# Optimization experiments

Measured on AMD Instinct MI355X. Metric: run time of the kernel, lower is better.

## Reference

```python
import jax, jax.numpy as jnp
import numpy as np

B, T, D = 4, 2048, 2048
HS, NH, NG = 128, 16, 4  # head_size, n_head, n_query_groups
R = NH // NG             # queries per group


def setup_inputs() -> dict:
    key = jax.random.key(0)
    ks = jax.random.split(key, 8)
    s = 0.02
    return {
        "x": jax.random.normal(ks[0], (B, T, D), dtype=jnp.float32),
        "WQ": jax.random.normal(ks[1], (HS * NH, D), dtype=jnp.float32) * s,
        "bQ": jax.random.normal(ks[2], (HS * NH,), dtype=jnp.float32) * s,
        "WK": jax.random.normal(ks[3], (HS * NG, D), dtype=jnp.float32) * s,
        "bK": jax.random.normal(ks[4], (HS * NG,), dtype=jnp.float32) * s,
        "WV": jax.random.normal(ks[5], (HS * NG, D), dtype=jnp.float32) * s,
        "bV": jax.random.normal(ks[6], (HS * NG,), dtype=jnp.float32) * s,
        "proj": jax.random.normal(ks[7], (HS * NH, D), dtype=jnp.float32) * s,
    }


def reference(x, WQ, bQ, WK, bK, WV, bV, proj):
    b, t, _ = x.shape
    # projections (torch Linear: x @ W.T + b)
    Q = x @ WQ.T + bQ                                   # (B,T,NH*HS)
    K = (x @ WK.T + bK).reshape(b, t, NG, HS)           # (B,T,NG,HS)
    V = (x @ WV.T + bV).reshape(b, t, NG, HS)
    # torch .repeat tiles the group axis: [g0..g3, g0..g3, ...]
    K = jnp.tile(K, (1, 1, R, 1)).reshape(b, t, NH * HS)
    V = jnp.tile(V, (1, 1, R, 1)).reshape(b, t, NH * HS)
    # single big-dim attention over the concatenated head dim (as in source)
    scores = jnp.einsum('btd,bsd->bts', Q, K)           # (B,T,T)
    causal = jnp.triu(jnp.ones((t, t), dtype=bool), 1)
    scores = jnp.where(causal[None], -jnp.inf, scores)
    # quirk: divide by sqrt(head_size) AFTER softmax
    attn = jax.nn.softmax(scores, axis=-1) / jnp.sqrt(jnp.float32(HS))
    Z = jnp.einsum('bts,bsd->btd', attn, V)             # (B,T,NH*HS)
    return Z @ proj                                     # (B,T,D)
```

## Files before the change

### kernel.cpp

```cpp
#include <hip/hip_runtime.h>
#include <math.h>

typedef _Float16 h16;
typedef _Float16 f16x8 __attribute__((ext_vector_type(8)));
typedef _Float16 f16x4 __attribute__((ext_vector_type(4)));
typedef float f32x4 __attribute__((ext_vector_type(4)));

enum { EPI_F32 = 0, EPI_SPLIT2 = 1, EPI_VT = 2, EPI_H16 = 3 };

struct GP {
  const h16* Ah; const h16* Al;
  const h16* Bh; const h16* Bl;
  const float* bias;
  float* outF;
  h16* oQh; h16* oQl; h16* oKh; h16* oKl;
  h16* outH;
  int K, lda, ldb, ldc;
  size_t sA, sB, sO;
};

__device__ __forceinline__ f32x4 mfma16(f16x8 a, f16x8 b, f32x4 c) {
  return __builtin_amdgcn_mfma_f32_16x16x32_f16(a, b, c, 0, 0, 0);
}

__device__ __forceinline__ void glds16(const h16* g, h16* l) {
  __builtin_amdgcn_global_load_lds((const __attribute__((address_space(1))) void*)g,
                                   (__attribute__((address_space(3))) void*)l,
                                   16, 0, 0);
}

template<int BM, int BN, int BSPL, int TERMS, int EPI, bool CSKIP, bool KLIM, bool DBUF>
__global__ __launch_bounds__(256, 2) void gemm_bt(GP p)
{
  constexpr int BK = 64;
  constexpr bool ASPL = (TERMS >= 2);
  constexpr int WM = BM / 2, WN = BN / 2;
  constexpr int FM = WM / 16, FN = WN / 16;
  constexpr int AH = BM * BK, BH = BN * BK;

  const int gx = gridDim.x, gy = gridDim.y;
  int lin = blockIdx.x + gx * blockIdx.y;
  const int nwg = gx * gy;
  if ((nwg & 7) == 0) lin = (lin & 7) * (nwg >> 3) + (lin >> 3);
  const int m0 = (lin / gx) * BM;
  const int n0 = (lin % gx) * BN;
  if (CSKIP && n0 >= m0 + BM) return;
  const int z = blockIdx.z;
  const h16* Ah = p.Ah + (size_t)z * p.sA;
  const h16* Al = ASPL ? p.Al + (size_t)z * p.sA : (const h16*)nullptr;
  const h16* Bh = p.Bh + (size_t)z * p.sB;
  const h16* Bl = BSPL ? p.Bl + (size_t)z * p.sB : (const h16*)nullptr;

  __shared__ h16 sAh[(DBUF ? 2 : 1) * AH];
  __shared__ h16 sAl[ASPL ? (DBUF ? 2 : 1) * AH : 8];
  __shared__ h16 sBh[(DBUF ? 2 : 1) * BH];
  __shared__ h16 sBl[BSPL ? (DBUF ? 2 : 1) * BH : 8];

  const int tid = threadIdx.x;
  const int lane = tid & 63;
  const int w = tid >> 6;
  const int wm = (w >> 1) * WM;
  const int wn = (w & 1) * WN;
  const int fr = lane & 15;
  const int fq = lane >> 4;
  const int lrow = lane >> 3;
  const int lcol = (((lane & 7) ^ lrow) * 8);

  f32x4 acc[FM][FN];
#pragma unroll
  for (int i = 0; i < FM; i++)
#pragma unroll
    for (int j = 0; j < FN; j++) acc[i][j] = f32x4{0.f, 0.f, 0.f, 0.f};

  const int kend = KLIM ? ((m0 + BM < p.K) ? (m0 + BM) : p.K) : p.K;

  auto stage = [&](int k0, int half) {
    const int ao = half * AH, bo = half * BH;
#pragma unroll
    for (int i = w; i < BM / 8; i += 4)
      glds16(Ah + (size_t)(m0 + i * 8 + lrow) * p.lda + (k0 + lcol), &sAh[ao + i * 512]);
    if constexpr (ASPL) {
#pragma unroll
      for (int i = w; i < BM / 8; i += 4)
        glds16(Al + (size_t)(m0 + i * 8 + lrow) * p.lda + (k0 + lcol), &sAl[ao + i * 512]);
    }
#pragma unroll
    for (int i = w; i < BN / 8; i += 4)
      glds16(Bh + (size_t)(n0 + i * 8 + lrow) * p.ldb + (k0 + lcol), &sBh[bo + i * 512]);
    if constexpr (BSPL) {
#pragma unroll
      for (int i = w; i < BN / 8; i += 4)
        glds16(Bl + (size_t)(n0 + i * 8 + lrow) * p.ldb + (k0 + lcol), &sBl[bo + i * 512]);
    }
  };

  auto compute = [&](int ca, int cb) {
#pragma unroll
    for (int ks = 0; ks < 2; ks++) {
      const int swo = (((ks * 4 + fq) ^ (fr & 7)) * 8);
      f16x8 fa[FM], fb[FN];
      f16x8 fal[ASPL ? FM : 1], fbl[BSPL ? FN : 1];
#pragma unroll
      for (int m = 0; m < FM; m++) {
        fa[m] = *(const f16x8*)&sAh[ca + (wm + m * 16 + fr) * BK + swo];
        if constexpr (ASPL)
          fal[m] = *(const f16x8*)&sAl[ca + (wm + m * 16 + fr) * BK + swo];
      }
#pragma unroll
      for (int n = 0; n < FN; n++) {
        fb[n] = *(const f16x8*)&sBh[cb + (wn + n * 16 + fr) * BK + swo];
        if constexpr (BSPL)
          fbl[n] = *(const f16x8*)&sBl[cb + (wn + n * 16 + fr) * BK + swo];
      }
#pragma unroll
      for (int m = 0; m < FM; m++)
#pragma unroll
        for (int n = 0; n < FN; n++) {
          acc[m][n] = mfma16(fa[m], fb[n], acc[m][n]);
          if constexpr (TERMS >= 2) acc[m][n] = mfma16(fal[m], fb[n], acc[m][n]);
          if constexpr (TERMS >= 3) acc[m][n] = mfma16(fa[m], fbl[n], acc[m][n]);
        }
    }
  };

  if constexpr (DBUF) {
    const int nIter = kend / BK;
    stage(0, 0);
    for (int it = 0; it < nIter; ++it) {
      __syncthreads();
      if (it + 1 < nIter) stage((it + 1) * BK, (it + 1) & 1);
      compute((it & 1) * AH, (it & 1) * BH);
    }
  } else {
    for (int k0 = 0; k0 < kend; k0 += BK) {
      __syncthreads();
      stage(k0, 0);
      __syncthreads();
      compute(0, 0);
    }
  }

#pragma unroll
  for (int m = 0; m < FM; m++) {
    const int grb = m0 + wm + m * 16 + fq * 4;
#pragma unroll
    for (int n = 0; n < FN; n++) {
      const int gc = n0 + wn + n * 16 + fr;
      if constexpr (EPI == EPI_F32) {
        float* o = p.outF + (size_t)z * p.sO;
#pragma unroll
        for (int r = 0; r < 4; r++)
          o[(size_t)(grb + r) * p.ldc + gc] = acc[m][n][r];
      } else if constexpr (EPI == EPI_SPLIT2) {
        const float bv = p.bias[gc];
#pragma unroll
        for (int r = 0; r < 4; r++) {
          const float v = acc[m][n][r] + bv;
          const h16 h = (h16)v;
          const h16 l = (h16)(v - (float)h);
          const size_t idx = (size_t)(grb + r) * 512;
          if (gc < 512) { p.oQh[idx + gc] = h; p.oQl[idx + gc] = l; }
          else          { p.oKh[idx + gc - 512] = h; p.oKl[idx + gc - 512] = l; }
        }
      } else if constexpr (EPI == EPI_VT) {
        const float bv = p.bias[gc];
        f16x4 pk;
#pragma unroll
        for (int r = 0; r < 4; r++) pk[r] = (h16)(acc[m][n][r] + bv);
        const int bb = grb >> 11;
        const int t  = grb & 2047;
        *(f16x4*)(p.outH + ((size_t)bb * 512 + gc) * 2048 + t) = pk;
      } else {
        h16* o = p.outH + (size_t)z * p.sO;
#pragma unroll
        for (int r = 0; r < 4; r++)
          o[(size_t)(grb + r) * p.ldc + gc] = (h16)acc[m][n][r];
      }
    }
  }
}

__global__ __launch_bounds__(256) void split_x(const float* __restrict__ x,
                                               h16* __restrict__ xh, h16* __restrict__ xl)
{
  const size_t i = ((size_t)blockIdx.x * 256 + threadIdx.x) * 8;
  const float4 a = *(const float4*)(x + i);
  const float4 b = *(const float4*)(x + i + 4);
  const float vv[8] = {a.x, a.y, a.z, a.w, b.x, b.y, b.z, b.w};
  f16x8 h, l;
#pragma unroll
  for (int j = 0; j < 8; j++) {
    const h16 hh = (h16)vv[j];
    h[j] = hh;
    l[j] = (h16)(vv[j] - (float)hh);
  }
  *(f16x8*)(xh + i) = h;
  *(f16x8*)(xl + i) = l;
}

__global__ __launch_bounds__(256) void softmax_row(const float* __restrict__ sc,
                                                   h16* __restrict__ attn)
{
  const int bt = blockIdx.x;
  const int t = bt & 2047;
  const int tid = threadIdx.x;
  const int lane = tid & 63;
  const int wid = tid >> 6;
  const int len = t + 1;
  const size_t rowoff = (size_t)bt * 2048;
  const float* row = sc + rowoff;
  const int c0 = tid * 8;
  const float4 a = *(const float4*)(row + c0);
  const float4 b = *(const float4*)(row + c0 + 4);
  float v[8] = {a.x, a.y, a.z, a.w, b.x, b.y, b.z, b.w};
#pragma unroll
  for (int j = 0; j < 8; j++)
    if (c0 + j >= len) v[j] = -INFINITY;
  float m = v[0];
#pragma unroll
  for (int j = 1; j < 8; j++) m = fmaxf(m, v[j]);
#pragma unroll
  for (int off = 32; off > 0; off >>= 1) m = fmaxf(m, __shfl_xor(m, off));
  __shared__ float redm[4];
  if (lane == 0) redm[wid] = m;
  __syncthreads();
  m = fmaxf(fmaxf(redm[0], redm[1]), fmaxf(redm[2], redm[3]));
  float e[8];
  float s = 0.f;
#pragma unroll
  for (int j = 0; j < 8; j++) { e[j] = expf(v[j] - m); s += e[j]; }
#pragma unroll
  for (int off = 32; off > 0; off >>= 1) s += __shfl_xor(s, off);
  __shared__ float reds[4];
  if (lane == 0) reds[wid] = s;
  __syncthreads();
  s = reds[0] + reds[1] + reds[2] + reds[3];
  const float inv = 1.f / (s * 11.313708498984761f);
  f16x8 o;
#pragma unroll
  for (int j = 0; j < 8; j++) o[j] = (h16)(e[j] * inv);
  *(f16x8*)(attn + rowoff + c0) = o;
}

__global__ __launch_bounds__(256) void prep_wqk(const float* __restrict__ WQ, const float* __restrict__ bQ,
                                                const float* __restrict__ WK, const float* __restrict__ bK,
                                                h16* __restrict__ Wh, h16* __restrict__ Wl,
                                                float* __restrict__ bias)
{
  const int idx = blockIdx.x * 256 + threadIdx.x;
  if (idx >= 1024 * 2048) return;
  const int n = idx >> 11;
  const int k = idx & 2047;
  float v;
  if (n < 512) {
    const int g = n >> 7, e = n & 127;
    const size_t base = (size_t)(128 * g + e) * 2048 + k;
    v = WQ[base] + WQ[base + (size_t)512 * 2048] + WQ[base + (size_t)1024 * 2048]
      + WQ[base + (size_t)1536 * 2048];
  } else {
    v = WK[(size_t)(n - 512) * 2048 + k];
  }
  const h16 h = (h16)v;
  Wh[idx] = h;
  Wl[idx] = (h16)(v - (float)h);
  if (k == 0) {
    if (n < 512) {
      const int g = n >> 7, e = n & 127;
      const int r = 128 * g + e;
      bias[n] = bQ[r] + bQ[r + 512] + bQ[r + 1024] + bQ[r + 1536];
    } else {
      bias[n] = bK[n - 512];
    }
  }
}

__global__ __launch_bounds__(256) void prep_wv(const float* __restrict__ WV, const float* __restrict__ bV,
                                               h16* __restrict__ Wv, float* __restrict__ bias)
{
  const int idx = blockIdx.x * 256 + threadIdx.x;
  if (idx >= 512 * 2048) return;
  Wv[idx] = (h16)WV[idx];
  if ((idx & 2047) == 0) bias[idx >> 11] = bV[idx >> 11];
}

__global__ __launch_bounds__(256) void prep_projT(const float* __restrict__ proj,
                                                  h16* __restrict__ projT)
{
  const int idx = blockIdx.x * 256 + threadIdx.x;
  if (idx >= 2048 * 512 / 4) return;
  const int n = idx >> 9;
  const int o = (idx & 511) << 2;
  const int g = n >> 7, e = n & 127;
  const size_t base = (size_t)(128 * g + e) * 2048 + o;
  const float4 a = *(const float4*)(proj + base);
  const float4 b = *(const float4*)(proj + base + (size_t)512 * 2048);
  const float4 c = *(const float4*)(proj + base + (size_t)1024 * 2048);
  const float4 d = *(const float4*)(proj + base + (size_t)1536 * 2048);
  projT[(size_t)(o + 0) * 512 + n] = (h16)(a.x + b.x + c.x + d.x);
  projT[(size_t)(o + 1) * 512 + n] = (h16)(a.y + b.y + c.y + d.y);
  projT[(size_t)(o + 2) * 512 + n] = (h16)(a.z + b.z + c.z + d.z);
  projT[(size_t)(o + 3) * 512 + n] = (h16)(a.w + b.w + c.w + d.w);
}

extern "C" void kernel_launch(void* const* d_in, const int* in_sizes, int n_in,
                              void* d_out, int out_size, void* d_ws, size_t ws_size,
                              hipStream_t stream)
{
  (void)in_sizes; (void)n_in;
  const float* x    = (const float*)d_in[0];
  const float* WQ   = (const float*)d_in[1];
  const float* bQv  = (const float*)d_in[2];
  const float* WK   = (const float*)d_in[3];
  const float* bKv  = (const float*)d_in[4];
  const float* WV   = (const float*)d_in[5];
  const float* bVv  = (const float*)d_in[6];
  const float* proj = (const float*)d_in[7];
  float* out = (float*)d_out;

  char* ws = (char*)d_ws;
  size_t off = 0;
  auto alloc = [&](size_t bytes) -> void* {
    off = (off + 255) & ~(size_t)255;
    void* p = ws + off;
    off += bytes;
    return p;
  };
  char* xregion = (char*)alloc((size_t)2 * 16777216 * 2);
  h16* xh = (h16*)xregion;
  h16* xl = (h16*)(xregion + (size_t)16777216 * 2);
  float* scores = (float*)xregion;
  h16* attn = (h16*)alloc((size_t)4 * 2048 * 2048 * 2);

  h16* Wqk_h = (h16*)alloc((size_t)1024 * 2048 * 2);
  h16* Wqk_l = (h16*)alloc((size_t)1024 * 2048 * 2);
  h16* Wv    = (h16*)alloc((size_t)512 * 2048 * 2);
  h16* projT = (h16*)alloc((size_t)2048 * 512 * 2);
  float* bias_qk = (float*)alloc(1024 * 4);
  float* bias_v  = (float*)alloc(512 * 4);
  h16* Qh = (h16*)alloc((size_t)8192 * 512 * 2);
  h16* Ql = (h16*)alloc((size_t)8192 * 512 * 2);
  h16* Kh = (h16*)alloc((size_t)8192 * 512 * 2);
  h16* Kl = (h16*)alloc((size_t)8192 * 512 * 2);
  h16* Vt = (h16*)alloc((size_t)4 * 512 * 2048 * 2);
  h16* Zg = (h16*)alloc((size_t)8192 * 512 * 2);
  if (off > ws_size) {
    hipMemsetAsync(d_out, 0x7F, (size_t)out_size * 4, stream);
    return;
  }

  prep_wqk<<<8192, 256, 0, stream>>>(WQ, bQv, WK, bKv, Wqk_h, Wqk_l, bias_qk);
  prep_wv<<<4096, 256, 0, stream>>>(WV, bVv, Wv, bias_v);
  prep_projT<<<1024, 256, 0, stream>>>(proj, projT);
  split_x<<<8192, 256, 0, stream>>>(x, xh, xl);

  {
    GP p{};
    p.Ah = xh; p.Al = xl; p.Bh = Wqk_h; p.Bl = Wqk_l; p.bias = bias_qk;
    p.oQh = Qh; p.oQl = Ql; p.oKh = Kh; p.oKl = Kl;
    p.K = 2048; p.lda = 2048; p.ldb = 2048; p.ldc = 0;
    gemm_bt<128, 128, 1, 3, EPI_SPLIT2, false, false, false><<<dim3(8, 64, 1), 256, 0, stream>>>(p);
  }
  {
    GP p{};
    p.Ah = xh; p.Bh = Wv; p.bias = bias_v; p.outH = Vt;
    p.K = 2048; p.lda = 2048; p.ldb = 2048; p.ldc = 0;
    gemm_bt<128, 64, 0, 1, EPI_VT, false, false, true><<<dim3(8, 64, 1), 256, 0, stream>>>(p);
  }
  {
    GP p{};
    p.Ah = Qh; p.Al = Ql; p.Bh = Kh; p.Bl = Kl; p.outF = scores;
    p.K = 512; p.lda = 512; p.ldb = 512; p.ldc = 2048;
    p.sA = (size_t)2048 * 512; p.sB = (size_t)2048 * 512; p.sO = (size_t)2048 * 2048;
    gemm_bt<128, 128, 1, 3, EPI_F32, true, false, false><<<dim3(16, 16, 4), 256, 0, stream>>>(p);
  }
  softmax_row<<<8192, 256, 0, stream>>>(scores, attn);
  {
    GP p{};
    p.Ah = attn; p.Bh = Vt; p.outH = Zg;
    p.K = 2048; p.lda = 2048; p.ldb = 2048; p.ldc = 512;
    p.sA = (size_t)2048 * 2048; p.sB = (size_t)512 * 2048; p.sO = (size_t)2048 * 512;
    gemm_bt<128, 64, 0, 1, EPI_H16, false, true, true><<<dim3(8, 16, 4), 256, 0, stream>>>(p);
  }
  {
    GP p{};
    p.Ah = Zg; p.Bh = projT; p.outF = out;
    p.K = 512; p.lda = 512; p.ldb = 512; p.ldc = 2048;
    gemm_bt<128, 128, 0, 1, EPI_F32, false, false, false><<<dim3(16, 64, 1), 256, 0, stream>>>(p);
  }
}
```

Measured before the change: 278.3 us.

## Pipeline split-precision GEMMs with BK=32 double buffering and trim softmax I/O

Adds a pipelined GEMM mode for the two 4-operand split-fp16 GEMMs (QK projection and scores). It uses BK=32 so the double-buffered tiles fit in LDS, adjusts the swizzle for that width, and uses explicit vmcnt waits so the next tile's global-to-LDS loads overlap compute. The softmax kernel skips loading score columns beyond the causal length and writes attention only up to the 128-aligned boundary that the KLIM PV GEMM reads. Risks include the hard-coded vmcnt count being wrong, smaller K steps raising loop overhead, and unwritten attn regions that rely on KLIM never reading them.

```diff
diff --git a/kernel.cpp b/kernel.cpp
--- a/kernel.cpp
+++ b/kernel.cpp
@@ -7,6 +7,7 @@
 typedef float f32x4 __attribute__((ext_vector_type(4)));
 
 enum { EPI_F32 = 0, EPI_SPLIT2 = 1, EPI_VT = 2, EPI_H16 = 3 };
+enum { M_SINGLE = 0, M_DBUF = 1, M_PIPE = 2 };
 
 struct GP {
   const h16* Ah; const h16* Al;
@@ -29,14 +30,18 @@
                                    16, 0, 0);
 }
 
-template<int BM, int BN, int BSPL, int TERMS, int EPI, bool CSKIP, bool KLIM, bool DBUF>
+template<int BM, int BN, int BK, int BSPL, int TERMS, int EPI, bool CSKIP, bool KLIM, int MODE>
 __global__ __launch_bounds__(256, 2) void gemm_bt(GP p)
 {
-  constexpr int BK = 64;
   constexpr bool ASPL = (TERMS >= 2);
   constexpr int WM = BM / 2, WN = BN / 2;
   constexpr int FM = WM / 16, FN = WN / 16;
   constexpr int AH = BM * BK, BH = BN * BK;
+  constexpr int LPR = BK / 8;
+  constexpr int RPG = 64 / LPR;
+  constexpr int NKS = BK / 32;
+  static_assert(MODE != M_PIPE || (BM == 128 && BN == 128 && BK == 32 && ASPL && BSPL),
+                "M_PIPE hard-codes vmcnt(8) for the 4-operand 128x128 BK=32 shape");
 
   const int gx = gridDim.x, gy = gridDim.y;
   int lin = blockIdx.x + gx * blockIdx.y;
@@ -51,10 +56,11 @@
   const h16* Bh = p.Bh + (size_t)z * p.sB;
   const h16* Bl = BSPL ? p.Bl + (size_t)z * p.sB : (const h16*)nullptr;
 
-  __shared__ h16 sAh[(DBUF ? 2 : 1) * AH];
-  __shared__ h16 sAl[ASPL ? (DBUF ? 2 : 1) * AH : 8];
-  __shared__ h16 sBh[(DBUF ? 2 : 1) * BH];
-  __shared__ h16 sBl[BSPL ? (DBUF ? 2 : 1) * BH : 8];
+  constexpr int NBUF = (MODE == M_SINGLE) ? 1 : 2;
+  __shared__ h16 sAh[NBUF * AH];
+  __shared__ h16 sAl[ASPL ? NBUF * AH : 8];
+  __shared__ h16 sBh[NBUF * BH];
+  __shared__ h16 sBl[BSPL ? NBUF * BH : 8];
 
   const int tid = threadIdx.x;
   const int lane = tid & 63;
@@ -63,8 +69,9 @@
   const int wn = (w & 1) * WN;
   const int fr = lane & 15;
   const int fq = lane >> 4;
-  const int lrow = lane >> 3;
-  const int lcol = (((lane & 7) ^ lrow) * 8);
+  const int lrow = lane / LPR;
+  const int lpos = lane % LPR;
+  const int lcol = (BK == 64 ? (lpos ^ lrow) : (lpos ^ ((lane >> 3) & 3))) * 8;
 
   f32x4 acc[FM][FN];
 #pragma unroll
@@ -77,27 +84,28 @@
   auto stage = [&](int k0, int half) {
     const int ao = half * AH, bo = half * BH;
 #pragma unroll
-    for (int i = w; i < BM / 8; i += 4)
-      glds16(Ah + (size_t)(m0 + i * 8 + lrow) * p.lda + (k0 + lcol), &sAh[ao + i * 512]);
+    for (int i = w; i < BM / RPG; i += 4)
+      glds16(Ah + (size_t)(m0 + i * RPG + lrow) * p.lda + (k0 + lcol), &sAh[ao + i * 512]);
     if constexpr (ASPL) {
 #pragma unroll
-      for (int i = w; i < BM / 8; i += 4)
-        glds16(Al + (size_t)(m0 + i * 8 + lrow) * p.lda + (k0 + lcol), &sAl[ao + i * 512]);
-    }
-#pragma unroll
-    for (int i = w; i < BN / 8; i += 4)
-      glds16(Bh + (size_t)(n0 + i * 8 + lrow) * p.ldb + (k0 + lcol), &sBh[bo + i * 512]);
+      for (int i = w; i < BM / RPG; i += 4)
+        glds16(Al + (size_t)(m0 + i * RPG + lrow) * p.lda + (k0 + lcol), &sAl[ao + i * 512]);
+    }
+#pragma unroll
+    for (int i = w; i < BN / RPG; i += 4)
+      glds16(Bh + (size_t)(n0 + i * RPG + lrow) * p.ldb + (k0 + lcol), &sBh[bo + i * 512]);
     if constexpr (BSPL) {
 #pragma unroll
-      for (int i = w; i < BN / 8; i += 4)
-        glds16(Bl + (size_t)(n0 + i * 8 + lrow) * p.ldb + (k0 + lcol), &sBl[bo + i * 512]);
+      for (int i = w; i < BN / RPG; i += 4)
+        glds16(Bl + (size_t)(n0 + i * RPG + lrow) * p.ldb + (k0 + lcol), &sBl[bo + i * 512]);
     }
   };
 
-  auto compute = [&](int ca, int cb) {
-#pragma unroll
-    for (int ks = 0; ks < 2; ks++) {
-      const int swo = (((ks * 4 + fq) ^ (fr & 7)) * 8);
+  auto compute = [&](int half) {
+    const int ca = half * AH, cb = half * BH;
+#pragma unroll
+    for (int ks = 0; ks < NKS; ks++) {
+      const int swo = (BK == 64 ? ((ks * 4 + fq) ^ (fr & 7)) : (fq ^ ((fr >> 1) & 3))) * 8;
       f16x8 fa[FM], fb[FN];
       f16x8 fal[ASPL ? FM : 1], fbl[BSPL ? FN : 1];
 #pragma unroll
@@ -123,20 +131,36 @@
     }
   };
 
-  if constexpr (DBUF) {
+  if constexpr (MODE == M_PIPE) {
+    const int nIter = kend / BK;
+    stage(0, 0);
+    for (int it = 0; it < nIter; ++it) {
+      asm volatile("s_waitcnt lgkmcnt(0)" ::: "memory");
+      __builtin_amdgcn_s_barrier();
+      if (it + 1 < nIter) {
+        stage((it + 1) * BK, (it + 1) & 1);
+        asm volatile("s_waitcnt vmcnt(8)" ::: "memory");
+      } else {
+        asm volatile("s_waitcnt vmcnt(0)" ::: "memory");
+      }
+      __builtin_amdgcn_s_barrier();
+      __builtin_amdgcn_sched_barrier(0);
+      compute(it & 1);
+    }
+  } else if constexpr (MODE == M_DBUF) {
     const int nIter = kend / BK;
     stage(0, 0);
     for (int it = 0; it < nIter; ++it) {
       __syncthreads();
       if (it + 1 < nIter) stage((it + 1) * BK, (it + 1) & 1);
-      compute((it & 1) * AH, (it & 1) * BH);
+      compute(it & 1);
     }
   } else {
     for (int k0 = 0; k0 < kend; k0 += BK) {
       __syncthreads();
       stage(k0, 0);
       __syncthreads();
-      compute(0, 0);
+      compute(0);
     }
   }
 
@@ -210,12 +234,19 @@
   const size_t rowoff = (size_t)bt * 2048;
   const float* row = sc + rowoff;
   const int c0 = tid * 8;
-  const float4 a = *(const float4*)(row + c0);
-  const float4 b = *(const float4*)(row + c0 + 4);
-  float v[8] = {a.x, a.y, a.z, a.w, b.x, b.y, b.z, b.w};
-#pragma unroll
-  for (int j = 0; j < 8; j++)
-    if (c0 + j >= len) v[j] = -INFINITY;
+  float v[8];
+  if (c0 < len) {
+    const float4 a = *(const float4*)(row + c0);
+    const float4 b = *(const float4*)(row + c0 + 4);
+    v[0] = a.x; v[1] = a.y; v[2] = a.z; v[3] = a.w;
+    v[4] = b.x; v[5] = b.y; v[6] = b.z; v[7] = b.w;
+#pragma unroll
+    for (int j = 0; j < 8; j++)
+      if (c0 + j >= len) v[j] = -INFINITY;
+  } else {
+#pragma unroll
+    for (int j = 0; j < 8; j++) v[j] = -INFINITY;
+  }
   float m = v[0];
 #pragma unroll
   for (int j = 1; j < 8; j++) m = fmaxf(m, v[j]);
@@ -236,10 +267,13 @@
   __syncthreads();
   s = reds[0] + reds[1] + reds[2] + reds[3];
   const float inv = 1.f / (s * 11.313708498984761f);
-  f16x8 o;
-#pragma unroll
-  for (int j = 0; j < 8; j++) o[j] = (h16)(e[j] * inv);
-  *(f16x8*)(attn + rowoff + c0) = o;
+  const int tend = ((t >> 7) + 1) << 7;
+  if (c0 < tend) {
+    f16x8 o;
+#pragma unroll
+    for (int j = 0; j < 8; j++) o[j] = (h16)(e[j] * inv);
+    *(f16x8*)(attn + rowoff + c0) = o;
+  }
 }
 
 __global__ __launch_bounds__(256) void prep_wqk(const float* __restrict__ WQ, const float* __restrict__ bQ,
@@ -358,20 +392,20 @@
     p.Ah = xh; p.Al = xl; p.Bh = Wqk_h; p.Bl = Wqk_l; p.bias = bias_qk;
     p.oQh = Qh; p.oQl = Ql; p.oKh = Kh; p.oKl = Kl;
     p.K = 2048; p.lda = 2048; p.ldb = 2048; p.ldc = 0;
-    gemm_bt<128, 128, 1, 3, EPI_SPLIT2, false, false, false><<<dim3(8, 64, 1), 256, 0, stream>>>(p);
+    gemm_bt<128, 128, 32, 1, 3, EPI_SPLIT2, false, false, M_PIPE><<<dim3(8, 64, 1), 256, 0, stream>>>(p);
   }
   {
     GP p{};
     p.Ah = xh; p.Bh = Wv; p.bias = bias_v; p.outH = Vt;
     p.K = 2048; p.lda = 2048; p.ldb = 2048; p.ldc = 0;
-    gemm_bt<128, 64, 0, 1, EPI_VT, false, false, true><<<dim3(8, 64, 1), 256, 0, stream>>>(p);
+    gemm_bt<128, 64, 64, 0, 1, EPI_VT, false, false, M_DBUF><<<dim3(8, 64, 1), 256, 0, stream>>>(p);
   }
   {
     GP p{};
     p.Ah = Qh; p.Al = Ql; p.Bh = Kh; p.Bl = Kl; p.outF = scores;
     p.K = 512; p.lda = 512; p.ldb = 512; p.ldc = 2048;
     p.sA = (size_t)2048 * 512; p.sB = (size_t)2048 * 512; p.sO = (size_t)2048 * 2048;
-    gemm_bt<128, 128, 1, 3, EPI_F32, true, false, false><<<dim3(16, 16, 4), 256, 0, stream>>>(p);
+    gemm_bt<128, 128, 32, 1, 3, EPI_F32, true, false, M_PIPE><<<dim3(16, 16, 4), 256, 0, stream>>>(p);
   }
   softmax_row<<<8192, 256, 0, stream>>>(scores, attn);
   {
@@ -379,12 +413,12 @@
     p.Ah = attn; p.Bh = Vt; p.outH = Zg;
     p.K = 2048; p.lda = 2048; p.ldb = 2048; p.ldc = 512;
     p.sA = (size_t)2048 * 2048; p.sB = (size_t)512 * 2048; p.sO = (size_t)2048 * 512;
-    gemm_bt<128, 64, 0, 1, EPI_H16, false, true, true><<<dim3(8, 16, 4), 256, 0, stream>>>(p);
+    gemm_bt<128, 64, 64, 0, 1, EPI_H16, false, true, M_DBUF><<<dim3(8, 16, 4), 256, 0, stream>>>(p);
   }
   {
     GP p{};
     p.Ah = Zg; p.Bh = projT; p.outF = out;
     p.K = 512; p.lda = 512; p.ldb = 512; p.ldc = 2048;
-    gemm_bt<128, 128, 0, 1, EPI_F32, false, false, false><<<dim3(16, 64, 1), 256, 0, stream>>>(p);
-  }
-}
+    gemm_bt<128, 128, 64, 0, 1, EPI_F32, false, false, M_SINGLE><<<dim3(16, 64, 1), 256, 0, stream>>>(p);
+  }
+}
```

Result: slower. 296.1 us (+6.4%).
